# Kernel optimization log

Measured on AMD Instinct MI355X. Metric: run time of the kernel, lower is better.

The kernel has to match this reference:

```python
import jax, jax.numpy as jnp
import numpy as np

DIM = 512
NUM_HEADS = 8
HEAD_DIM = DIM // NUM_HEADS
EPS = 1e-6


def setup_inputs() -> dict:
    key = jax.random.key(0)
    k_x, k_qkv, k_out, k_b = jax.random.split(key, 4)
    B, N = 8, 4096
    x = jax.random.normal(k_x, (B, N, DIM), dtype=jnp.float32)
    # nn.Linear weights stored as [out_features, in_features]; we keep [in, out] for x @ W
    s_qkv = 1.0 / np.sqrt(DIM)
    W_qkv = jax.random.uniform(k_qkv, (DIM, 3 * DIM), minval=-s_qkv, maxval=s_qkv, dtype=jnp.float32)
    W_out = jax.random.uniform(k_out, (DIM, DIM), minval=-s_qkv, maxval=s_qkv, dtype=jnp.float32)
    b_out = jax.random.uniform(k_b, (DIM,), minval=-s_qkv, maxval=s_qkv, dtype=jnp.float32)
    return {"x": x, "W_qkv": W_qkv, "W_out": W_out, "b_out": b_out}


def _feature_map(x):
    # elu(x) + 1
    return jax.nn.elu(x) + 1.0


def reference(x, W_qkv, W_out, b_out):
    B, N, C = x.shape
    H, D = NUM_HEADS, HEAD_DIM
    qkv = x @ W_qkv                              # [B, N, 3C]
    qkv = qkv.reshape(B, N, 3, H, D).transpose(2, 0, 3, 1, 4)  # [3, B, H, N, D]
    q, k, v = qkv[0], qkv[1], qkv[2]
    q_phi = _feature_map(q)                      # [B, H, N, D]
    k_phi = _feature_map(k)
    KV = jnp.einsum('bhnd,bhne->bhde', k_phi, v)  # [B, H, D, D]
    K_sum = k_phi.sum(axis=2)                     # [B, H, D]
    denom = jnp.einsum('bhnd,bhd->bhn', q_phi, K_sum)[..., None] + EPS  # [B, H, N, 1]
    out = jnp.einsum('bhnd,bhde->bhne', q_phi, KV) / denom              # [B, H, N, D]
    out = out.transpose(0, 2, 1, 3).reshape(B, N, C)
    return out @ W_out + b_out
```

## Files before the change

### kernel.cpp

```cpp
#include <hip/hip_runtime.h>
#include <stdint.h>

typedef float    f32x4 __attribute__((ext_vector_type(4)));
typedef short    s16x8 __attribute__((ext_vector_type(8)));
typedef short    s16x4 __attribute__((ext_vector_type(4)));
typedef unsigned short u16;
typedef uint32_t u32;

#define DEVINL __device__ __forceinline__

DEVINL float bf2f(u16 u) { union { u32 i; float f; } x; x.i = ((u32)u) << 16; return x.f; }
DEVINL u16 f2bf(float f) {
  union { float f; u32 i; } x; x.f = f;
  u32 i = x.i;
  return (u16)((i + 0x7FFFu + ((i >> 16) & 1u)) >> 16);
}

DEVINL void gload16(const void* g, void* l) {
  __builtin_amdgcn_global_load_lds((const __attribute__((address_space(1))) void*)g,
                                   (__attribute__((address_space(3))) void*)l,
                                   16, 0, 0);
}

__global__ __launch_bounds__(256) void k_conv_bf16(const float* __restrict__ x,
                                                   u16* __restrict__ xb, int n8) {
  int stride = gridDim.x * blockDim.x;
  for (int i = blockIdx.x * blockDim.x + threadIdx.x; i < n8; i += stride) {
    const f32x4* p = (const f32x4*)(x + (size_t)i * 8);
    f32x4 a = p[0], b = p[1];
    s16x8 o;
    o[0] = (short)f2bf(a[0]); o[1] = (short)f2bf(a[1]);
    o[2] = (short)f2bf(a[2]); o[3] = (short)f2bf(a[3]);
    o[4] = (short)f2bf(b[0]); o[5] = (short)f2bf(b[1]);
    o[6] = (short)f2bf(b[2]); o[7] = (short)f2bf(b[3]);
    *(s16x8*)(xb + (size_t)i * 8) = o;
  }
}

__global__ __launch_bounds__(256) void k_transpose_bf16(const float* __restrict__ W,
                                                        u16* __restrict__ Wt, int K, int N) {
  __shared__ __align__(16) float t[64][65];
  int nb = N >> 6;
  int tn = blockIdx.x % nb, tk = blockIdx.x / nb;
  int n0 = tn << 6, k0 = tk << 6;
  int tid = threadIdx.x;
  int cr = tid >> 4, cc = (tid & 15) << 2;
#pragma unroll
  for (int i = 0; i < 4; i++) {
    int r = cr + (i << 4);
    f32x4 v = *(const f32x4*)(W + (size_t)(k0 + r) * N + n0 + cc);
    t[r][cc] = v[0]; t[r][cc + 1] = v[1]; t[r][cc + 2] = v[2]; t[r][cc + 3] = v[3];
  }
  __syncthreads();
#pragma unroll
  for (int i = 0; i < 4; i++) {
    int nn = cr + (i << 4);
    s16x4 o;
    o[0] = (short)f2bf(t[cc    ][nn]);
    o[1] = (short)f2bf(t[cc + 1][nn]);
    o[2] = (short)f2bf(t[cc + 2][nn]);
    o[3] = (short)f2bf(t[cc + 3][nn]);
    *(s16x4*)(Wt + (size_t)(n0 + nn) * K + k0 + cc) = o;
  }
}

template <int EPI>
__global__ __launch_bounds__(512, 1) void k_gemm(
    const u16* __restrict__ A, const u16* __restrict__ Bt,
    int nbn,
    u16* __restrict__ qph, u16* __restrict__ kph, u16* __restrict__ vv,
    float* __restrict__ out, const float* __restrict__ bias) {
  __shared__ __align__(16) u16 lsA[2][256 * 64];
  __shared__ __align__(16) u16 lsB[2][256 * 64];

  int nwg = gridDim.x;
  int bx = blockIdx.x;
  int o = (bx & 7) * (nwg >> 3) + (bx >> 3);
  int bm = o / nbn, bn = o % nbn;
  int m0 = bm << 8, n0 = bn << 8;
  int tid = threadIdx.x;
  int w = tid >> 6, lane = tid & 63;
  int lnlo = lane & 15, lnhi = lane >> 4;
  int wr = w >> 2, wc = w & 3;

  const u16* gAp[4]; const u16* gBp[4]; int ldst[4];
#pragma unroll
  for (int i = 0; i < 4; i++) {
    int c = tid + i * 512;
    int row = c >> 3, chl = c & 7;
    int gch = chl ^ (row & 7);
    gAp[i] = A + (size_t)(m0 + row) * 512 + gch * 8;
    gBp[i] = Bt + (size_t)(n0 + row) * 512 + gch * 8;
    ldst[i] = c * 8;
  }

  int offA[2][8], offB[2][4];
#pragma unroll
  for (int ks = 0; ks < 2; ks++) {
#pragma unroll
    for (int f = 0; f < 8; f++) {
      int r = wr * 128 + f * 16 + lnlo;
      offA[ks][f] = (r * 8 + ((ks * 4 + lnhi) ^ (r & 7))) * 8;
    }
#pragma unroll
    for (int f = 0; f < 4; f++) {
      int r = wc * 64 + f * 16 + lnlo;
      offB[ks][f] = (r * 8 + ((ks * 4 + lnhi) ^ (r & 7))) * 8;
    }
  }

  auto stage = [&](int t) {
    int par = t & 1, k0 = t * 64;
#pragma unroll
    for (int i = 0; i < 4; i++) gload16(gAp[i] + k0, &lsA[par][ldst[i]]);
#pragma unroll
    for (int i = 0; i < 4; i++) gload16(gBp[i] + k0, &lsB[par][ldst[i]]);
  };

  f32x4 acc[8][4] = {};

  stage(0);
  asm volatile("s_waitcnt vmcnt(0)" ::: "memory");
  __builtin_amdgcn_s_barrier();

  for (int t = 0; t < 8; t++) {
    int par = t & 1;
    if (t < 7) stage(t + 1);
    const u16* La = &lsA[par][0];
    const u16* Lb = &lsB[par][0];
#pragma unroll
    for (int ks = 0; ks < 2; ks++) {
      s16x8 af[8], bf[4];
#pragma unroll
      for (int f = 0; f < 8; f++) af[f] = *(const s16x8*)(La + offA[ks][f]);
#pragma unroll
      for (int f = 0; f < 4; f++) bf[f] = *(const s16x8*)(Lb + offB[ks][f]);
      __builtin_amdgcn_s_setprio(1);
#pragma unroll
      for (int mf = 0; mf < 8; mf++)
#pragma unroll
        for (int nf = 0; nf < 4; nf++)
          acc[mf][nf] = __builtin_amdgcn_mfma_f32_16x16x32_bf16(af[mf], bf[nf], acc[mf][nf], 0, 0, 0);
      __builtin_amdgcn_s_setprio(0);
    }
    if (t < 7) {
      asm volatile("s_waitcnt vmcnt(0)" ::: "memory");
      __builtin_amdgcn_s_barrier();
    }
  }

  int gmB = m0 + wr * 128;
  int gnB = n0 + wc * 64;
  if (EPI == 0) {
#pragma unroll
    for (int mf = 0; mf < 8; mf++) {
#pragma unroll
      for (int nf = 0; nf < 4; nf++) {
        int col = gnB + nf * 16 + lnlo;
        int sec = col >> 9;
        int hh = (col >> 6) & 7;
        int dd = col & 63;
        u16* dst = (sec == 0) ? qph : ((sec == 1) ? kph : vv);
#pragma unroll
        for (int r = 0; r < 4; r++) {
          int rowm = gmB + mf * 16 + lnhi * 4 + r;
          float val = acc[mf][nf][r];
          if (sec < 2) val = (val > 0.f) ? (val + 1.f) : __expf(val);
          int bidx = rowm >> 12, tok = rowm & 4095;
          dst[(((size_t)(bidx * 8 + hh) * 4096 + tok) << 6) + dd] = f2bf(val);
        }
      }
    }
  } else {
#pragma unroll
    for (int mf = 0; mf < 8; mf++) {
#pragma unroll
      for (int nf = 0; nf < 4; nf++) {
        int col = gnB + nf * 16 + lnlo;
        float bv = bias[col];
#pragma unroll
        for (int r = 0; r < 4; r++) {
          int rowm = gmB + mf * 16 + lnhi * 4 + r;
          out[(size_t)rowm * 512 + col] = acc[mf][nf][r] + bv;
        }
      }
    }
  }
}

__global__ __launch_bounds__(256) void k_kv(const u16* __restrict__ kphi,
                                            const u16* __restrict__ vbuf,
                                            float* __restrict__ kvpart,
                                            float* __restrict__ kspart) {
  __shared__ __align__(16) float kf[16][64];
  __shared__ __align__(16) float vf[16][64];
  int bx = blockIdx.x;
  int bh = bx >> 4, ck = bx & 15;
  int tid = threadIdx.x;
  size_t base = ((size_t)bh * 4096 + ck * 256) * 64;
  float acc[4][4] = {};
  float ks[4] = {0.f, 0.f, 0.f, 0.f};
  int dq = tid >> 4, eq = tid & 15;
  int d0 = dq * 4, e0 = eq * 4;
  int half = tid >> 7;
  int t2 = tid & 127;
  int srow = t2 >> 3, sch = t2 & 7;

  for (int step = 0; step < 16; step++) {
    {
      const u16* src = (half ? vbuf : kphi) + base + (size_t)(step * 16 + srow) * 64 + sch * 8;
      s16x8 v8 = *(const s16x8*)src;
      float* dst = (half ? &vf[0][0] : &kf[0][0]) + srow * 64 + sch * 8;
      f32x4 lo = {bf2f((u16)v8[0]), bf2f((u16)v8[1]), bf2f((u16)v8[2]), bf2f((u16)v8[3])};
      f32x4 hi = {bf2f((u16)v8[4]), bf2f((u16)v8[5]), bf2f((u16)v8[6]), bf2f((u16)v8[7])};
      *(f32x4*)dst = lo;
      *(f32x4*)(dst + 4) = hi;
    }
    __syncthreads();
#pragma unroll
    for (int tk = 0; tk < 16; tk++) {
      f32x4 kq = *(const f32x4*)&kf[tk][d0];
      f32x4 vq = *(const f32x4*)&vf[tk][e0];
#pragma unroll
      for (int i = 0; i < 4; i++)
#pragma unroll
        for (int j = 0; j < 4; j++) acc[i][j] += kq[i] * vq[j];
      if (eq == 0) {
#pragma unroll
        for (int i = 0; i < 4; i++) ks[i] += kq[i];
      }
    }
    __syncthreads();
  }
  size_t pb = (size_t)(bh * 16 + ck) * 4096;
#pragma unroll
  for (int i = 0; i < 4; i++) {
    f32x4 o = {acc[i][0], acc[i][1], acc[i][2], acc[i][3]};
    *(f32x4*)(kvpart + pb + (size_t)(d0 + i) * 64 + e0) = o;
  }
  if (eq == 0) {
    f32x4 o = {ks[0], ks[1], ks[2], ks[3]};
    *(f32x4*)(kspart + (size_t)(bh * 16 + ck) * 64 + d0) = o;
  }
}

__global__ __launch_bounds__(256) void k_kvred(const float* __restrict__ kvpart,
                                               const float* __restrict__ kspart,
                                               u16* __restrict__ kvt_sw,
                                               float* __restrict__ ksum) {
  int bh = blockIdx.x;
  int tid = threadIdx.x;
  int e = tid >> 2, d0 = (tid & 3) * 16;
  size_t pb = (size_t)bh * 16 * 4096;
#pragma unroll
  for (int dd = 0; dd < 16; dd++) {
    int d = d0 + dd;
    float s = 0.f;
#pragma unroll
    for (int c = 0; c < 16; c++) s += kvpart[pb + (size_t)c * 4096 + d * 64 + e];
    int chs = (d >> 3) ^ (e & 7);
    kvt_sw[((size_t)bh * 64 + e) * 64 + chs * 8 + (d & 7)] = f2bf(s);
  }
  if (tid < 64) {
    float s = 0.f;
#pragma unroll
    for (int c = 0; c < 16; c++) s += kspart[(size_t)bh * 1024 + c * 64 + tid];
    ksum[bh * 64 + tid] = s;
  }
}

__global__ __launch_bounds__(256, 2) void k_attnout(const u16* __restrict__ qphi,
                                                    const u16* __restrict__ kvt_sw,
                                                    const float* __restrict__ ksum,
                                                    u16* __restrict__ y) {
  __shared__ __align__(16) u16 qa[256 * 64];
  __shared__ __align__(16) u16 bb[64 * 64];
  __shared__ float ksl[64];
  __shared__ float rdnl[256];
  int bx = blockIdx.x;
  int bh = bx >> 4, tch = bx & 15;
  int b = bh >> 3, hh = bh & 7;
  int tid = threadIdx.x, w = tid >> 6, lane = tid & 63;
  int lnlo = lane & 15, lnhi = lane >> 4;
  size_t qbase = ((size_t)bh * 4096 + tch * 256) * 64;

#pragma unroll
  for (int i = 0; i < 8; i++) {
    int c = i * 256 + tid;
    int row = c >> 3, ch = c & 7;
    int gcol = (ch ^ (row & 7)) << 3;
    gload16(qphi + qbase + (size_t)row * 64 + gcol, &qa[c * 8]);
  }
#pragma unroll
  for (int i = 0; i < 2; i++) {
    int c = i * 256 + tid;
    gload16(kvt_sw + (size_t)bh * 4096 + c * 8, &bb[c * 8]);
  }
  if (tid < 64) ksl[tid] = ksum[bh * 64 + tid];
  __syncthreads();

  {
    float den = 0.f;
#pragma unroll
    for (int ch = 0; ch < 8; ch++) {
      s16x8 v8 = *(const s16x8*)&qa[tid * 64 + ((ch ^ (tid & 7)) << 3)];
#pragma unroll
      for (int j = 0; j < 8; j++) den += bf2f((u16)v8[j]) * ksl[ch * 8 + j];
    }
    rdnl[tid] = 1.f / (den + 1e-6f);
  }
  __syncthreads();

  f32x4 acc[4][4] = {};
#pragma unroll
  for (int kk = 0; kk < 2; kk++) {
    s16x8 af[4], bfr[4];
#pragma unroll
    for (int f = 0; f < 4; f++) {
      int ra = w * 64 + f * 16 + lnlo;
      int ca = (kk * 4 + lnhi) ^ (ra & 7);
      af[f] = *(const s16x8*)&qa[ra * 64 + ca * 8];
      int rb = f * 16 + lnlo;
      int cb = (kk * 4 + lnhi) ^ (rb & 7);
      bfr[f] = *(const s16x8*)&bb[rb * 64 + cb * 8];
    }
#pragma unroll
    for (int mf = 0; mf < 4; mf++)
#pragma unroll
      for (int nf = 0; nf < 4; nf++)
        acc[mf][nf] = __builtin_amdgcn_mfma_f32_16x16x32_bf16(af[mf], bfr[nf], acc[mf][nf], 0, 0, 0);
  }

  size_t yrow0 = (size_t)b * 4096 + tch * 256;
#pragma unroll
  for (int mf = 0; mf < 4; mf++) {
#pragma unroll
    for (int nf = 0; nf < 4; nf++) {
      int e = nf * 16 + lnlo;
#pragma unroll
      for (int r = 0; r < 4; r++) {
        int tl = w * 64 + mf * 16 + lnhi * 4 + r;
        float val = acc[mf][nf][r] * rdnl[tl];
        y[(yrow0 + tl) * 512 + hh * 64 + e] = f2bf(val);
      }
    }
  }
}

#define OFF_XB     ((size_t)0)
#define OFF_WQKVT  ((size_t)33554432)
#define OFF_WOUTT  ((size_t)35127296)
#define OFF_QPHI   ((size_t)35651584)
#define OFF_KPHI   ((size_t)69206016)
#define OFF_VBUF   ((size_t)102760448)
#define OFF_KVPART ((size_t)136314880)
#define OFF_KSPART ((size_t)153092096)
#define OFF_KVT    ((size_t)153354240)
#define OFF_KSUM   ((size_t)153878528)

extern "C" void kernel_launch(void* const* d_in, const int* in_sizes, int n_in,
                              void* d_out, int out_size, void* d_ws, size_t ws_size,
                              hipStream_t stream) {
  const float* x    = (const float*)d_in[0];
  const float* Wqkv = (const float*)d_in[1];
  const float* Wout = (const float*)d_in[2];
  const float* bout = (const float*)d_in[3];
  float* out = (float*)d_out;
  char* ws = (char*)d_ws;

  u16* xb     = (u16*)(ws + OFF_XB);
  u16* y      = (u16*)(ws + OFF_XB);
  u16* wqkvt  = (u16*)(ws + OFF_WQKVT);
  u16* woutt  = (u16*)(ws + OFF_WOUTT);
  u16* qphi   = (u16*)(ws + OFF_QPHI);
  u16* kphi   = (u16*)(ws + OFF_KPHI);
  u16* vbuf   = (u16*)(ws + OFF_VBUF);
  float* kvpart = (float*)(ws + OFF_KVPART);
  float* kspart = (float*)(ws + OFF_KSPART);
  u16* kvt_sw = (u16*)(ws + OFF_KVT);
  float* ksum = (float*)(ws + OFF_KSUM);

  k_conv_bf16<<<2048, 256, 0, stream>>>(x, xb, 16777216 / 8);
  k_transpose_bf16<<<(1536 / 64) * (512 / 64), 256, 0, stream>>>(Wqkv, wqkvt, 512, 1536);
  k_transpose_bf16<<<(512 / 64) * (512 / 64), 256, 0, stream>>>(Wout, woutt, 512, 512);

  k_gemm<0><<<768, 512, 0, stream>>>(xb, wqkvt, 6, qphi, kphi, vbuf, nullptr, nullptr);
  k_kv<<<64 * 16, 256, 0, stream>>>(kphi, vbuf, kvpart, kspart);
  k_kvred<<<64, 256, 0, stream>>>(kvpart, kspart, kvt_sw, ksum);
  k_attnout<<<64 * 16, 256, 0, stream>>>(qphi, kvt_sw, ksum, y);
  k_gemm<1><<<256, 512, 0, stream>>>(y, woutt, 2, nullptr, nullptr, nullptr, out, bout);
}
```

Before: 184.7 us.

## Triple-buffer GEMM K-loop with 32-wide tiles and interleaved load/MFMA phases

Replaces the double-buffered 64-wide K staging with a three-stage ring of 32-wide K tiles, prefetching two tiles ahead. Each iteration splits the MFMA work into two half-phases, interleaving the global-to-LDS loads of A and B with the compute. Partial vmcnt waits replace full drains so loads overlap more with math. This adds more barriers per K-step and a new swizzle pattern for the narrower tiles, which risks bank conflicts or extra sync overhead.

```diff
diff --git a/kernel.cpp b/kernel.cpp
--- a/kernel.cpp
+++ b/kernel.cpp
@@ -70,8 +70,8 @@
     int nbn,
     u16* __restrict__ qph, u16* __restrict__ kph, u16* __restrict__ vv,
     float* __restrict__ out, const float* __restrict__ bias) {
-  __shared__ __align__(16) u16 lsA[2][256 * 64];
-  __shared__ __align__(16) u16 lsB[2][256 * 64];
+  __shared__ __align__(16) u16 lsA[3][256 * 32];
+  __shared__ __align__(16) u16 lsB[3][256 * 32];
 
   int nwg = gridDim.x;
   int bx = blockIdx.x;
@@ -83,70 +83,87 @@
   int lnlo = lane & 15, lnhi = lane >> 4;
   int wr = w >> 2, wc = w & 3;
 
-  const u16* gAp[4]; const u16* gBp[4]; int ldst[4];
-#pragma unroll
-  for (int i = 0; i < 4; i++) {
+  const u16* gAp[2]; const u16* gBp[2]; int ldst[2];
+#pragma unroll
+  for (int i = 0; i < 2; i++) {
     int c = tid + i * 512;
-    int row = c >> 3, chl = c & 7;
-    int gch = chl ^ (row & 7);
+    int row = c >> 2, ch = c & 3;
+    int gch = ch ^ ((row >> 1) & 3);
     gAp[i] = A + (size_t)(m0 + row) * 512 + gch * 8;
     gBp[i] = Bt + (size_t)(n0 + row) * 512 + gch * 8;
     ldst[i] = c * 8;
   }
 
-  int offA[2][8], offB[2][4];
-#pragma unroll
-  for (int ks = 0; ks < 2; ks++) {
-#pragma unroll
-    for (int f = 0; f < 8; f++) {
-      int r = wr * 128 + f * 16 + lnlo;
-      offA[ks][f] = (r * 8 + ((ks * 4 + lnhi) ^ (r & 7))) * 8;
-    }
-#pragma unroll
-    for (int f = 0; f < 4; f++) {
-      int r = wc * 64 + f * 16 + lnlo;
-      offB[ks][f] = (r * 8 + ((ks * 4 + lnhi) ^ (r & 7))) * 8;
-    }
-  }
-
-  auto stage = [&](int t) {
-    int par = t & 1, k0 = t * 64;
-#pragma unroll
-    for (int i = 0; i < 4; i++) gload16(gAp[i] + k0, &lsA[par][ldst[i]]);
-#pragma unroll
-    for (int i = 0; i < 4; i++) gload16(gBp[i] + k0, &lsB[par][ldst[i]]);
-  };
+  int offA[8], offB[4];
+#pragma unroll
+  for (int f = 0; f < 8; f++) {
+    int r = wr * 128 + f * 16 + lnlo;
+    offA[f] = r * 32 + (lnhi ^ ((r >> 1) & 3)) * 8;
+  }
+#pragma unroll
+  for (int f = 0; f < 4; f++) {
+    int r = wc * 64 + f * 16 + lnlo;
+    offB[f] = r * 32 + (lnhi ^ ((r >> 1) & 3)) * 8;
+  }
 
   f32x4 acc[8][4] = {};
 
-  stage(0);
-  asm volatile("s_waitcnt vmcnt(0)" ::: "memory");
+#pragma unroll
+  for (int i = 0; i < 2; i++) gload16(gAp[i], &lsA[0][ldst[i]]);
+#pragma unroll
+  for (int i = 0; i < 2; i++) gload16(gBp[i], &lsB[0][ldst[i]]);
+#pragma unroll
+  for (int i = 0; i < 2; i++) gload16(gAp[i] + 32, &lsA[1][ldst[i]]);
+#pragma unroll
+  for (int i = 0; i < 2; i++) gload16(gBp[i] + 32, &lsB[1][ldst[i]]);
+  asm volatile("s_waitcnt vmcnt(4)" ::: "memory");
   __builtin_amdgcn_s_barrier();
 
-  for (int t = 0; t < 8; t++) {
-    int par = t & 1;
-    if (t < 7) stage(t + 1);
-    const u16* La = &lsA[par][0];
-    const u16* Lb = &lsB[par][0];
-#pragma unroll
-    for (int ks = 0; ks < 2; ks++) {
-      s16x8 af[8], bf[4];
-#pragma unroll
-      for (int f = 0; f < 8; f++) af[f] = *(const s16x8*)(La + offA[ks][f]);
-#pragma unroll
-      for (int f = 0; f < 4; f++) bf[f] = *(const s16x8*)(Lb + offB[ks][f]);
-      __builtin_amdgcn_s_setprio(1);
-#pragma unroll
-      for (int mf = 0; mf < 8; mf++)
-#pragma unroll
-        for (int nf = 0; nf < 4; nf++)
-          acc[mf][nf] = __builtin_amdgcn_mfma_f32_16x16x32_bf16(af[mf], bf[nf], acc[mf][nf], 0, 0, 0);
-      __builtin_amdgcn_s_setprio(0);
-    }
-    if (t < 7) {
-      asm volatile("s_waitcnt vmcnt(0)" ::: "memory");
-      __builtin_amdgcn_s_barrier();
-    }
+#pragma unroll
+  for (int t = 0; t < 16; t++) {
+    int buf = t % 3;
+    const u16* La = &lsA[buf][0];
+    const u16* Lb = &lsB[buf][0];
+    int k2 = (t + 2) * 32;
+    int b2 = (t + 2) % 3;
+
+    s16x8 bf[4], af[4];
+#pragma unroll
+    for (int f = 0; f < 4; f++) bf[f] = *(const s16x8*)(Lb + offB[f]);
+#pragma unroll
+    for (int f = 0; f < 4; f++) af[f] = *(const s16x8*)(La + offA[f]);
+    if (t < 14) {
+#pragma unroll
+      for (int i = 0; i < 2; i++) gload16(gAp[i] + k2, &lsA[b2][ldst[i]]);
+    }
+    __builtin_amdgcn_s_barrier();
+    __builtin_amdgcn_s_setprio(1);
+#pragma unroll
+    for (int mf = 0; mf < 4; mf++)
+#pragma unroll
+      for (int nf = 0; nf < 4; nf++)
+        acc[mf][nf] = __builtin_amdgcn_mfma_f32_16x16x32_bf16(af[mf], bf[nf], acc[mf][nf], 0, 0, 0);
+    __builtin_amdgcn_s_setprio(0);
+    __builtin_amdgcn_s_barrier();
+
+    s16x8 af2[4];
+#pragma unroll
+    for (int f = 0; f < 4; f++) af2[f] = *(const s16x8*)(La + offA[4 + f]);
+    if (t < 14) {
+#pragma unroll
+      for (int i = 0; i < 2; i++) gload16(gBp[i] + k2, &lsB[b2][ldst[i]]);
+    }
+    __builtin_amdgcn_s_barrier();
+    __builtin_amdgcn_s_setprio(1);
+#pragma unroll
+    for (int mf = 0; mf < 4; mf++)
+#pragma unroll
+      for (int nf = 0; nf < 4; nf++)
+        acc[4 + mf][nf] = __builtin_amdgcn_mfma_f32_16x16x32_bf16(af2[mf], bf[nf], acc[4 + mf][nf], 0, 0, 0);
+    __builtin_amdgcn_s_setprio(0);
+    if (t <= 13)      asm volatile("s_waitcnt vmcnt(4)" ::: "memory");
+    else if (t == 14) asm volatile("s_waitcnt vmcnt(0)" ::: "memory");
+    if (t < 15) __builtin_amdgcn_s_barrier();
   }
 
   int gmB = m0 + wr * 128;
```

Measured after the change: 178.5 us. 1.03x faster.

## Restructure GEMM to 128x256 tiles with B fragments streamed from global into registers

Applied to the files above, without the earlier changes.

The GEMM kernel now uses 256-thread blocks with 128x256 output tiles and a 32-wide k-step. Only A is staged in LDS, with a smaller swizzled double buffer. Each wave loads its B fragments straight from global memory into double-buffered registers, and blocks are ordered so consecutive blocks share the same B columns. The intent is to cut LDS footprint and traffic, allow two blocks per CU, and overlap loads with MFMA work, at the cost of more global B reads and twice as many barriers per k. Separately, the k_kv inner loop is regrouped to load four rows of k and v before doing the FMAs.

```diff
diff --git a/kernel.cpp b/kernel.cpp
--- a/kernel.cpp
+++ b/kernel.cpp
@@ -8,6 +8,7 @@
 typedef uint32_t u32;
 
 #define DEVINL __device__ __forceinline__
+#define CFENCE asm volatile("" ::: "memory")
 
 DEVINL float bf2f(u16 u) { union { u32 i; float f; } x; x.i = ((u32)u) << 16; return x.f; }
 DEVINL u16 f2bf(float f) {
@@ -65,92 +66,88 @@
 }
 
 template <int EPI>
-__global__ __launch_bounds__(512, 1) void k_gemm(
+__global__ __launch_bounds__(256, 2) void k_gemm(
     const u16* __restrict__ A, const u16* __restrict__ Bt,
-    int nbn,
+    int nbm,
     u16* __restrict__ qph, u16* __restrict__ kph, u16* __restrict__ vv,
     float* __restrict__ out, const float* __restrict__ bias) {
-  __shared__ __align__(16) u16 lsA[2][256 * 64];
-  __shared__ __align__(16) u16 lsB[2][256 * 64];
-
-  int nwg = gridDim.x;
-  int bx = blockIdx.x;
+  __shared__ __align__(16) u16 lsA[2][128 * 32];
+
+  int nwg = gridDim.x, bx = blockIdx.x;
   int o = (bx & 7) * (nwg >> 3) + (bx >> 3);
-  int bm = o / nbn, bn = o % nbn;
-  int m0 = bm << 8, n0 = bn << 8;
-  int tid = threadIdx.x;
-  int w = tid >> 6, lane = tid & 63;
+  int bn = o / nbm, bm = o % nbm;
+  int m0 = bm << 7, n0 = bn << 8;
+  int tid = threadIdx.x, w = tid >> 6, lane = tid & 63;
   int lnlo = lane & 15, lnhi = lane >> 4;
-  int wr = w >> 2, wc = w & 3;
-
-  const u16* gAp[4]; const u16* gBp[4]; int ldst[4];
-#pragma unroll
-  for (int i = 0; i < 4; i++) {
-    int c = tid + i * 512;
-    int row = c >> 3, chl = c & 7;
-    int gch = chl ^ (row & 7);
-    gAp[i] = A + (size_t)(m0 + row) * 512 + gch * 8;
-    gBp[i] = Bt + (size_t)(n0 + row) * 512 + gch * 8;
-    ldst[i] = c * 8;
-  }
-
-  int offA[2][8], offB[2][4];
-#pragma unroll
-  for (int ks = 0; ks < 2; ks++) {
-#pragma unroll
-    for (int f = 0; f < 8; f++) {
-      int r = wr * 128 + f * 16 + lnlo;
-      offA[ks][f] = (r * 8 + ((ks * 4 + lnhi) ^ (r & 7))) * 8;
-    }
-#pragma unroll
-    for (int f = 0; f < 4; f++) {
-      int r = wc * 64 + f * 16 + lnlo;
-      offB[ks][f] = (r * 8 + ((ks * 4 + lnhi) ^ (r & 7))) * 8;
-    }
-  }
-
-  auto stage = [&](int t) {
-    int par = t & 1, k0 = t * 64;
-#pragma unroll
-    for (int i = 0; i < 4; i++) gload16(gAp[i] + k0, &lsA[par][ldst[i]]);
-#pragma unroll
-    for (int i = 0; i < 4; i++) gload16(gBp[i] + k0, &lsB[par][ldst[i]]);
+
+  const u16* gA0; const u16* gA1; int ldst0, ldst1;
+  {
+    int c = tid, row = c >> 2, ch = c & 3;
+    gA0 = A + (size_t)(m0 + row) * 512 + (ch ^ ((row >> 1) & 3)) * 8;
+    ldst0 = c * 8;
+    c = tid + 256; row = c >> 2; ch = c & 3;
+    gA1 = A + (size_t)(m0 + row) * 512 + (ch ^ ((row >> 1) & 3)) * 8;
+    ldst1 = c * 8;
+  }
+  const u16* gB[4];
+#pragma unroll
+  for (int nf = 0; nf < 4; nf++)
+    gB[nf] = Bt + (size_t)(n0 + w * 64 + nf * 16 + lnlo) * 512 + lnhi * 8;
+  int offA[8];
+#pragma unroll
+  for (int mf = 0; mf < 8; mf++) {
+    int r = mf * 16 + lnlo;
+    offA[mf] = r * 32 + (lnhi ^ ((r >> 1) & 3)) * 8;
+  }
+
+  f32x4 acc[8][4] = {};
+  s16x8 rB0[4], rB1[4];
+
+  gload16(gA0, &lsA[0][ldst0]);
+  gload16(gA1, &lsA[0][ldst1]);
+  CFENCE;
+#pragma unroll
+  for (int nf = 0; nf < 4; nf++) rB0[nf] = *(const s16x8*)gB[nf];
+  CFENCE;
+  asm volatile("s_waitcnt vmcnt(4)" ::: "memory");
+  __builtin_amdgcn_s_barrier();
+  CFENCE;
+
+  auto tile = [&](int t, s16x8 (&rcur)[4], s16x8 (&rnxt)[4]) {
+    const int par = t & 1;
+    if (t < 15) {
+      int k1 = (t + 1) * 32;
+      gload16(gA0 + k1, &lsA[par ^ 1][ldst0]);
+      gload16(gA1 + k1, &lsA[par ^ 1][ldst1]);
+      CFENCE;
+#pragma unroll
+      for (int nf = 0; nf < 4; nf++) rnxt[nf] = *(const s16x8*)(gB[nf] + k1);
+      CFENCE;
+    }
+    s16x8 af[8];
+#pragma unroll
+    for (int mf = 0; mf < 8; mf++) af[mf] = *(const s16x8*)&lsA[par][offA[mf]];
+    __builtin_amdgcn_s_setprio(1);
+#pragma unroll
+    for (int mf = 0; mf < 8; mf++)
+#pragma unroll
+      for (int nf = 0; nf < 4; nf++)
+        acc[mf][nf] = __builtin_amdgcn_mfma_f32_16x16x32_bf16(af[mf], rcur[nf], acc[mf][nf], 0, 0, 0);
+    __builtin_amdgcn_s_setprio(0);
+    if (t < 15) {
+      asm volatile("s_waitcnt vmcnt(4)" ::: "memory");
+      __builtin_amdgcn_s_barrier();
+      CFENCE;
+    }
   };
 
-  f32x4 acc[8][4] = {};
-
-  stage(0);
-  asm volatile("s_waitcnt vmcnt(0)" ::: "memory");
-  __builtin_amdgcn_s_barrier();
-
-  for (int t = 0; t < 8; t++) {
-    int par = t & 1;
-    if (t < 7) stage(t + 1);
-    const u16* La = &lsA[par][0];
-    const u16* Lb = &lsB[par][0];
-#pragma unroll
-    for (int ks = 0; ks < 2; ks++) {
-      s16x8 af[8], bf[4];
-#pragma unroll
-      for (int f = 0; f < 8; f++) af[f] = *(const s16x8*)(La + offA[ks][f]);
-#pragma unroll
-      for (int f = 0; f < 4; f++) bf[f] = *(const s16x8*)(Lb + offB[ks][f]);
-      __builtin_amdgcn_s_setprio(1);
-#pragma unroll
-      for (int mf = 0; mf < 8; mf++)
-#pragma unroll
-        for (int nf = 0; nf < 4; nf++)
-          acc[mf][nf] = __builtin_amdgcn_mfma_f32_16x16x32_bf16(af[mf], bf[nf], acc[mf][nf], 0, 0, 0);
-      __builtin_amdgcn_s_setprio(0);
-    }
-    if (t < 7) {
-      asm volatile("s_waitcnt vmcnt(0)" ::: "memory");
-      __builtin_amdgcn_s_barrier();
-    }
-  }
-
-  int gmB = m0 + wr * 128;
-  int gnB = n0 + wc * 64;
+#pragma unroll
+  for (int t = 0; t < 16; t += 2) {
+    tile(t, rB0, rB1);
+    tile(t + 1, rB1, rB0);
+  }
+
+  int gnB = n0 + w * 64;
   if (EPI == 0) {
 #pragma unroll
     for (int mf = 0; mf < 8; mf++) {
@@ -163,7 +160,7 @@
         u16* dst = (sec == 0) ? qph : ((sec == 1) ? kph : vv);
 #pragma unroll
         for (int r = 0; r < 4; r++) {
-          int rowm = gmB + mf * 16 + lnhi * 4 + r;
+          int rowm = m0 + mf * 16 + lnhi * 4 + r;
           float val = acc[mf][nf][r];
           if (sec < 2) val = (val > 0.f) ? (val + 1.f) : __expf(val);
           int bidx = rowm >> 12, tok = rowm & 4095;
@@ -180,7 +177,7 @@
         float bv = bias[col];
 #pragma unroll
         for (int r = 0; r < 4; r++) {
-          int rowm = gmB + mf * 16 + lnhi * 4 + r;
+          int rowm = m0 + mf * 16 + lnhi * 4 + r;
           out[(size_t)rowm * 512 + col] = acc[mf][nf][r] + bv;
         }
       }
@@ -218,16 +215,23 @@
     }
     __syncthreads();
 #pragma unroll
-    for (int tk = 0; tk < 16; tk++) {
-      f32x4 kq = *(const f32x4*)&kf[tk][d0];
-      f32x4 vq = *(const f32x4*)&vf[tk][e0];
-#pragma unroll
-      for (int i = 0; i < 4; i++)
-#pragma unroll
-        for (int j = 0; j < 4; j++) acc[i][j] += kq[i] * vq[j];
-      if (eq == 0) {
-#pragma unroll
-        for (int i = 0; i < 4; i++) ks[i] += kq[i];
+    for (int tkb = 0; tkb < 4; tkb++) {
+      f32x4 kq[4], vq[4];
+#pragma unroll
+      for (int j = 0; j < 4; j++) {
+        kq[j] = *(const f32x4*)&kf[tkb * 4 + j][d0];
+        vq[j] = *(const f32x4*)&vf[tkb * 4 + j][e0];
+      }
+#pragma unroll
+      for (int j = 0; j < 4; j++) {
+#pragma unroll
+        for (int i = 0; i < 4; i++)
+#pragma unroll
+          for (int l = 0; l < 4; l++) acc[i][l] += kq[j][i] * vq[j][l];
+        if (eq == 0) {
+#pragma unroll
+          for (int i = 0; i < 4; i++) ks[i] += kq[j][i];
+        }
       }
     }
     __syncthreads();
@@ -235,12 +239,12 @@
   size_t pb = (size_t)(bh * 16 + ck) * 4096;
 #pragma unroll
   for (int i = 0; i < 4; i++) {
-    f32x4 o = {acc[i][0], acc[i][1], acc[i][2], acc[i][3]};
-    *(f32x4*)(kvpart + pb + (size_t)(d0 + i) * 64 + e0) = o;
+    f32x4 oo = {acc[i][0], acc[i][1], acc[i][2], acc[i][3]};
+    *(f32x4*)(kvpart + pb + (size_t)(d0 + i) * 64 + e0) = oo;
   }
   if (eq == 0) {
-    f32x4 o = {ks[0], ks[1], ks[2], ks[3]};
-    *(f32x4*)(kspart + (size_t)(bh * 16 + ck) * 64 + d0) = o;
+    f32x4 oo = {ks[0], ks[1], ks[2], ks[3]};
+    *(f32x4*)(kspart + (size_t)(bh * 16 + ck) * 64 + d0) = oo;
   }
 }
 
@@ -384,9 +388,9 @@
   k_transpose_bf16<<<(1536 / 64) * (512 / 64), 256, 0, stream>>>(Wqkv, wqkvt, 512, 1536);
   k_transpose_bf16<<<(512 / 64) * (512 / 64), 256, 0, stream>>>(Wout, woutt, 512, 512);
 
-  k_gemm<0><<<768, 512, 0, stream>>>(xb, wqkvt, 6, qphi, kphi, vbuf, nullptr, nullptr);
+  k_gemm<0><<<1536, 256, 0, stream>>>(xb, wqkvt, 256, qphi, kphi, vbuf, nullptr, nullptr);
   k_kv<<<64 * 16, 256, 0, stream>>>(kphi, vbuf, kvpart, kspart);
   k_kvred<<<64, 256, 0, stream>>>(kvpart, kspart, kvt_sw, ksum);
   k_attnout<<<64 * 16, 256, 0, stream>>>(qphi, kvt_sw, ksum, y);
-  k_gemm<1><<<256, 512, 0, stream>>>(y, woutt, 2, nullptr, nullptr, nullptr, out, bout);
-}
+  k_gemm<1><<<512, 256, 0, stream>>>(y, woutt, 256, nullptr, nullptr, nullptr, out, bout);
+}
```

Result: slower. 196.5 us (+6.4%).
